# Kernel tuning notes

Hardware: AMD Instinct MI355X
Metric: run time of the kernel (lower is better)

Reference implementation:

```python
import jax, jax.numpy as jnp
import numpy as np

N_SRC = 50000
N_DST = 50000
E = 800000
IN_DIM = 128
OUT_DIM = 64
HEADS = 4
NEG_SLOPE = 0.2  # PyG GATConv default negative_slope
EPS = 1e-16      # PyG softmax denominator epsilon


def setup_inputs() -> dict:
    key = jax.random.key(0)
    ks = jax.random.split(key, 8)
    x_src = jax.random.normal(ks[0], (N_SRC, IN_DIM), dtype=jnp.float32)
    x_dst = jax.random.normal(ks[1], (N_DST, IN_DIM), dtype=jnp.float32)
    src = jax.random.randint(ks[2], (E,), 0, N_SRC, dtype=jnp.int32)
    dst = jax.random.randint(ks[3], (E,), 0, N_DST, dtype=jnp.int32)
    edge_index = jnp.stack([src, dst], axis=0)
    W_src = jax.random.normal(ks[4], (IN_DIM, HEADS * OUT_DIM), dtype=jnp.float32) / np.sqrt(IN_DIM)
    W_dst = jax.random.normal(ks[5], (IN_DIM, HEADS * OUT_DIM), dtype=jnp.float32) / np.sqrt(IN_DIM)
    att_src = jax.random.normal(ks[6], (HEADS, OUT_DIM), dtype=jnp.float32) / np.sqrt(OUT_DIM)
    att_dst = jax.random.normal(ks[7], (HEADS, OUT_DIM), dtype=jnp.float32) / np.sqrt(OUT_DIM)
    bias = jnp.zeros((OUT_DIM,), dtype=jnp.float32)
    return {"x_src": x_src, "x_dst": x_dst, "edge_index": edge_index,
            "W_src": W_src, "W_dst": W_dst, "att_src": att_src,
            "att_dst": att_dst, "bias": bias}


def reference(x_src, x_dst, edge_index, W_src, W_dst, att_src, att_dst, bias):
    # Linear projections -> [N, H, C]
    hs = (x_src @ W_src).reshape(N_SRC, HEADS, OUT_DIM)
    hd = (x_dst @ W_dst).reshape(N_DST, HEADS, OUT_DIM)
    # Per-node attention logits -> [N, H]
    a_s = jnp.einsum('nhc,hc->nh', hs, att_src)
    a_d = jnp.einsum('nhc,hc->nh', hd, att_dst)

    src, dst = edge_index[0], edge_index[1]
    # Per-edge logits [E, H]
    alpha = jax.nn.leaky_relu(a_s[src] + a_d[dst], negative_slope=NEG_SLOPE)
    # Segment softmax over edges sharing the same dst node
    amax = jax.ops.segment_max(alpha, dst, num_segments=N_DST)
    alpha = jnp.exp(alpha - amax[dst])
    denom = jax.ops.segment_sum(alpha, dst, num_segments=N_DST)
    alpha = alpha / (denom[dst] + EPS)
    # (dropout=0 / eval mode: no attention dropout)
    # Message + scatter-add aggregation: out[i] = sum_e alpha_e * hs[src_e]
    msg = hs[src] * alpha[:, :, None]                 # [E, H, C]
    out = jax.ops.segment_sum(msg, dst, num_segments=N_DST)  # [N_dst, H, C]
    # concat=False -> mean over heads, then bias
    return out.mean(axis=1) + bias
```

## Files before the change

kernel.cpp:

```cpp
#include <hip/hip_runtime.h>
#include <hip/hip_bf16.h>

#define N_SRC 50000
#define N_DST 50000
#define NEDGE 800000
#define IND   128
#define HEADS 4
#define CDIM  64
#define HC    256
#define MAXDEG 96
#define NB_ALPHA 12500
#define NB_HIST  3125

typedef _Float16 half8  __attribute__((ext_vector_type(8)));
typedef _Float16 half2t __attribute__((ext_vector_type(2)));
typedef float    f32x4  __attribute__((ext_vector_type(4)));

static __device__ __forceinline__ unsigned int pack2h(float a, float b) {
    union { half2t h; unsigned int u; } v;
    v.h[0] = (_Float16)a; v.h[1] = (_Float16)b;
    return v.u;
}
static __device__ __forceinline__ half2t bits2h(unsigned int u) {
    union { unsigned int u; half2t h; } v; v.u = u; return v.h;
}

__global__ void prep_kernel(const float* __restrict__ Wdst,
                            const float* __restrict__ att_d,
                            float* __restrict__ WdA,
                            const float* __restrict__ Wsrc,
                            _Float16* __restrict__ WhT, int* __restrict__ deg) {
    int b = blockIdx.x, tid = threadIdx.x;
    if (b < 196) {
        int i = b * 256 + tid;
        if (i < N_DST) deg[i] = 0;
    } else if (b < 198) {
        int id = (b - 196) * 256 + tid;
        int k = id >> 2, h = id & 3;
        float acc = 0.f;
        for (int c = 0; c < CDIM; ++c)
            acc += Wdst[k * HC + h * CDIM + c] * att_d[h * CDIM + c];
        WdA[id] = acc;
    } else {
        int idx = (b - 198) * 256 + tid;
        int n = idx >> 7, k = idx & 127;
        WhT[idx] = (_Float16)Wsrc[k * HC + n];
    }
}

__global__ __launch_bounds__(256) void gemm_mfma_kernel(
        const float* __restrict__ x, const _Float16* __restrict__ WhT,
        const float* __restrict__ att_s,
        unsigned short* __restrict__ hsTh, float* __restrict__ a_s) {
    int tid = threadIdx.x;
    int w = tid >> 6, lane = tid & 63;
    int ll = lane & 15, q = lane >> 4;
    int rbase = blockIdx.x * 64 + w * 16;

    int arow = rbase + ll;
    if (arow >= N_SRC) arow = N_SRC - 1;
    const float* xr = x + (size_t)arow * IND + q * 8;
    half8 afrag[4];
    #pragma unroll
    for (int kf = 0; kf < 4; ++kf) {
        float4 u0 = *(const float4*)(xr + kf * 32);
        float4 u1 = *(const float4*)(xr + kf * 32 + 4);
        half8 a;
        a[0] = (_Float16)u0.x; a[1] = (_Float16)u0.y;
        a[2] = (_Float16)u0.z; a[3] = (_Float16)u0.w;
        a[4] = (_Float16)u1.x; a[5] = (_Float16)u1.y;
        a[6] = (_Float16)u1.z; a[7] = (_Float16)u1.w;
        afrag[kf] = a;
    }

    f32x4 acc[16];
    #pragma unroll
    for (int t = 0; t < 16; ++t) acc[t] = (f32x4){0.f, 0.f, 0.f, 0.f};

    #pragma unroll
    for (int t = 0; t < 16; ++t) {
        const _Float16* bp = WhT + (size_t)(t * 16 + ll) * IND + q * 8;
        half8 b0 = *(const half8*)(bp + 0);
        half8 b1 = *(const half8*)(bp + 32);
        half8 b2 = *(const half8*)(bp + 64);
        half8 b3 = *(const half8*)(bp + 96);
        f32x4 c = acc[t];
        c = __builtin_amdgcn_mfma_f32_16x16x32_f16(afrag[0], b0, c, 0, 0, 0);
        c = __builtin_amdgcn_mfma_f32_16x16x32_f16(afrag[1], b1, c, 0, 0, 0);
        c = __builtin_amdgcn_mfma_f32_16x16x32_f16(afrag[2], b2, c, 0, 0, 0);
        c = __builtin_amdgcn_mfma_f32_16x16x32_f16(afrag[3], b3, c, 0, 0, 0);
        acc[t] = c;
    }

    #pragma unroll
    for (int tg = 0; tg < 4; ++tg) {
        #pragma unroll
        for (int r = 0; r < 4; ++r) {
            int n = rbase + q * 4 + r;
            if (n < N_SRC) {
                uint2 v;
                v.x = pack2h(acc[tg     ][r], acc[tg + 4 ][r]);
                v.y = pack2h(acc[tg + 8 ][r], acc[tg + 12][r]);
                *(uint2*)(hsTh + (size_t)n * HC + (tg * 16 + ll) * 4) = v;
            }
        }
    }

    float attv[16];
    #pragma unroll
    for (int t = 0; t < 16; ++t) attv[t] = att_s[t * 16 + ll];
    #pragma unroll
    for (int r = 0; r < 4; ++r) {
        float4 p;
        p.x = acc[0][r]*attv[0]  + acc[1][r]*attv[1]  + acc[2][r]*attv[2]  + acc[3][r]*attv[3];
        p.y = acc[4][r]*attv[4]  + acc[5][r]*attv[5]  + acc[6][r]*attv[6]  + acc[7][r]*attv[7];
        p.z = acc[8][r]*attv[8]  + acc[9][r]*attv[9]  + acc[10][r]*attv[10]+ acc[11][r]*attv[11];
        p.w = acc[12][r]*attv[12]+ acc[13][r]*attv[13]+ acc[14][r]*attv[14]+ acc[15][r]*attv[15];
        #pragma unroll
        for (int off = 1; off < 16; off <<= 1) {
            p.x += __shfl_xor(p.x, off, 64);
            p.y += __shfl_xor(p.y, off, 64);
            p.z += __shfl_xor(p.z, off, 64);
            p.w += __shfl_xor(p.w, off, 64);
        }
        int n = rbase + q * 4 + r;
        if (ll == 0 && n < N_SRC) *(float4*)(a_s + (size_t)n * 4) = p;
    }
}

__global__ __launch_bounds__(256) void mid_kernel(
        const float* __restrict__ x_dst, const float* __restrict__ WdA,
        float* __restrict__ a_d,
        const int* __restrict__ src, const int* __restrict__ dst,
        int* __restrict__ deg, int* __restrict__ col2) {
    int b = blockIdx.x, tid = threadIdx.x;
    if (b < NB_ALPHA) {
        int n    = (b * 256 + tid) >> 6;
        int lane = tid & 63;
        const float* xp = x_dst + (size_t)n * IND;
        const float4* wa = (const float4*)WdA;
        float x0 = xp[lane], x1 = xp[lane + 64];
        float4 wa0 = wa[lane], wa1 = wa[lane + 64];
        float p0 = x0 * wa0.x + x1 * wa1.x;
        float p1 = x0 * wa0.y + x1 * wa1.y;
        float p2 = x0 * wa0.z + x1 * wa1.z;
        float p3 = x0 * wa0.w + x1 * wa1.w;
        for (int off = 32; off >= 1; off >>= 1) {
            p0 += __shfl_xor(p0, off, 64);
            p1 += __shfl_xor(p1, off, 64);
            p2 += __shfl_xor(p2, off, 64);
            p3 += __shfl_xor(p3, off, 64);
        }
        if (lane == 0) {
            a_d[n * 4 + 0] = p0; a_d[n * 4 + 1] = p1;
            a_d[n * 4 + 2] = p2; a_d[n * 4 + 3] = p3;
        }
    } else {
        int e = (b - NB_ALPHA) * 256 + tid;
        if (e < NEDGE) {
            int d = dst[e];
            int r = atomicAdd(&deg[d], 1);
            if (r < MAXDEG) col2[d * MAXDEG + r] = src[e];
        }
    }
}

__global__ __launch_bounds__(256) void aggregate_kernel(
        const int* __restrict__ deg, const int* __restrict__ col2,
        const float4* __restrict__ as4, const float4* __restrict__ ad4,
        const unsigned short* __restrict__ hsTh,
        const float* __restrict__ bias, float* __restrict__ out) {
    __shared__ int   s_off[4][MAXDEG];
    __shared__ uint4 s_pk[4][MAXDEG];
    int tid = threadIdx.x;
    int wv = tid >> 6, lane = tid & 63;
    int i = (blockIdx.x * 256 + tid) >> 6;
    if (i >= N_DST) return;
    int dg = deg[i]; if (dg > MAXDEG) dg = MAXDEG;
    float bv = bias[lane];
    if (dg == 0) { out[i * CDIM + lane] = bv; return; }
    float4 ad = ad4[i];
    const int* crow = col2 + i * MAXDEG;

    float s0 = 0.f, s1 = 0.f, s2 = 0.f, s3 = 0.f;
    for (int e = lane; e < dg; e += 64) {
        int sn = crow[e];
        float4 av = as4[sn];
        float lx = av.x + ad.x; lx = lx > 0.f ? lx : 0.2f * lx;
        float ly = av.y + ad.y; ly = ly > 0.f ? ly : 0.2f * ly;
        float lz = av.z + ad.z; lz = lz > 0.f ? lz : 0.2f * lz;
        float lw = av.w + ad.w; lw = lw > 0.f ? lw : 0.2f * lw;
        float w0 = __expf(lx), w1 = __expf(ly), w2 = __expf(lz), w3 = __expf(lw);
        s0 += w0; s1 += w1; s2 += w2; s3 += w3;
        s_off[wv][e] = sn * HC;
        float4 wf = {w0, w1, w2, w3};
        *(float4*)&s_pk[wv][e] = wf;
    }
    for (int off = 32; off >= 1; off >>= 1) {
        s0 += __shfl_xor(s0, off, 64);
        s1 += __shfl_xor(s1, off, 64);
        s2 += __shfl_xor(s2, off, 64);
        s3 += __shfl_xor(s3, off, 64);
    }
    float i0 = 0.25f / (s0 + 1e-16f);
    float i1 = 0.25f / (s1 + 1e-16f);
    float i2 = 0.25f / (s2 + 1e-16f);
    float i3 = 0.25f / (s3 + 1e-16f);

    for (int e = lane; e < dg; e += 64) {
        float4 wf = *(float4*)&s_pk[wv][e];
        uint4 pk;
        pk.x = (unsigned int)s_off[wv][e];
        pk.y = pack2h(wf.x * i0, wf.y * i1);
        pk.z = pack2h(wf.z * i2, wf.w * i3);
        pk.w = 0;
        s_pk[wv][e] = pk;
    }
    __asm__ volatile("s_waitcnt lgkmcnt(0)" ::: "memory");

    const unsigned short* hb = hsTh + (lane << 2);
    float acc = 0.f;
    int j = 0;
    for (; j + 4 <= dg; j += 4) {
        uint4 p0 = s_pk[wv][j];
        uint4 p1 = s_pk[wv][j + 1];
        uint4 p2 = s_pk[wv][j + 2];
        uint4 p3 = s_pk[wv][j + 3];
        uint2 h0 = *(const uint2*)(hb + p0.x);
        uint2 h1 = *(const uint2*)(hb + p1.x);
        uint2 h2 = *(const uint2*)(hb + p2.x);
        uint2 h3 = *(const uint2*)(hb + p3.x);
        acc = __builtin_amdgcn_fdot2(bits2h(h0.x), bits2h(p0.y), acc, false);
        acc = __builtin_amdgcn_fdot2(bits2h(h0.y), bits2h(p0.z), acc, false);
        acc = __builtin_amdgcn_fdot2(bits2h(h1.x), bits2h(p1.y), acc, false);
        acc = __builtin_amdgcn_fdot2(bits2h(h1.y), bits2h(p1.z), acc, false);
        acc = __builtin_amdgcn_fdot2(bits2h(h2.x), bits2h(p2.y), acc, false);
        acc = __builtin_amdgcn_fdot2(bits2h(h2.y), bits2h(p2.z), acc, false);
        acc = __builtin_amdgcn_fdot2(bits2h(h3.x), bits2h(p3.y), acc, false);
        acc = __builtin_amdgcn_fdot2(bits2h(h3.y), bits2h(p3.z), acc, false);
    }
    for (; j < dg; ++j) {
        uint4 p0 = s_pk[wv][j];
        uint2 h0 = *(const uint2*)(hb + p0.x);
        acc = __builtin_amdgcn_fdot2(bits2h(h0.x), bits2h(p0.y), acc, false);
        acc = __builtin_amdgcn_fdot2(bits2h(h0.y), bits2h(p0.z), acc, false);
    }
    out[i * CDIM + lane] = acc + bv;
}

extern "C" void kernel_launch(void* const* d_in, const int* in_sizes, int n_in,
                              void* d_out, int out_size, void* d_ws, size_t ws_size,
                              hipStream_t stream) {
    const float* x_src   = (const float*)d_in[0];
    const float* x_dst   = (const float*)d_in[1];
    const int*   ei      = (const int*)d_in[2];
    const float* W_src   = (const float*)d_in[3];
    const float* W_dst   = (const float*)d_in[4];
    const float* att_src = (const float*)d_in[5];
    const float* att_dst = (const float*)d_in[6];
    const float* bias    = (const float*)d_in[7];
    float* out = (float*)d_out;

    char* ws = (char*)d_ws;
    unsigned short* hsTh = (unsigned short*)ws; ws += (size_t)N_SRC * HC * 2;
    int*    col2    = (int*)ws;    ws += (size_t)N_DST * MAXDEG * 4;
    float*  a_s     = (float*)ws;  ws += (size_t)N_SRC * 4 * 4;
    float*  a_d     = (float*)ws;  ws += (size_t)N_DST * 4 * 4;
    float*  WdA     = (float*)ws;  ws += 2048;
    _Float16* WhT   = (_Float16*)ws; ws += IND * HC * 2;
    int*    deg     = (int*)ws;    ws += N_DST * 4;

    prep_kernel<<<326, 256, 0, stream>>>(W_dst, att_dst, WdA, W_src, WhT, deg);
    gemm_mfma_kernel<<<(N_SRC + 63) / 64, 256, 0, stream>>>(x_src, WhT, att_src, hsTh, a_s);
    mid_kernel<<<NB_ALPHA + NB_HIST, 256, 0, stream>>>(x_dst, WdA, a_d, ei, ei + NEDGE, deg, col2);
    aggregate_kernel<<<(N_DST + 3) / 4, 256, 0, stream>>>(deg, col2,
                                                          (const float4*)a_s, (const float4*)a_d,
                                                          hsTh, bias, out);
}
```

Before: 251.5 us.

## Fuse GEMM with alpha/histogram kernel, partition scatter by dst range, shrink col indices

Merges the source-projection GEMM and the dst-logit/bucketing kernel into one launch, which removes a launch and lets the two phases overlap. The edge bucketing is split into 8 dst-range partitions: every edge chunk is read 8 times, but each block only touches one eighth of the deg/col arrays, so the scattered atomics and stores stay more local in cache. Column indices are stored as 16-bit values, halving the bucket footprint. The aggregate kernel orders its blocks to match the partitions. The a_d computation now does two nodes per wave. The risk is the 8x redundant reading of dst indices.

```diff
diff --git a/kernel.cpp b/kernel.cpp
--- a/kernel.cpp
+++ b/kernel.cpp
@@ -9,8 +9,12 @@
 #define CDIM  64
 #define HC    256
 #define MAXDEG 96
-#define NB_ALPHA 12500
-#define NB_HIST  3125
+#define NDST8 6250
+
+#define NB_GEMM  782
+#define NB_ALPHA 6250
+#define NB_HIST  25000
+#define NB_AGG   (1563 * 8)
 
 typedef _Float16 half8  __attribute__((ext_vector_type(8)));
 typedef _Float16 half2t __attribute__((ext_vector_type(2)));
@@ -48,125 +52,126 @@
     }
 }
 
-__global__ __launch_bounds__(256) void gemm_mfma_kernel(
-        const float* __restrict__ x, const _Float16* __restrict__ WhT,
+__global__ __launch_bounds__(256) void fused_kernel(
+        const float* __restrict__ x_src, const _Float16* __restrict__ WhT,
         const float* __restrict__ att_s,
-        unsigned short* __restrict__ hsTh, float* __restrict__ a_s) {
-    int tid = threadIdx.x;
-    int w = tid >> 6, lane = tid & 63;
-    int ll = lane & 15, q = lane >> 4;
-    int rbase = blockIdx.x * 64 + w * 16;
-
-    int arow = rbase + ll;
-    if (arow >= N_SRC) arow = N_SRC - 1;
-    const float* xr = x + (size_t)arow * IND + q * 8;
-    half8 afrag[4];
-    #pragma unroll
-    for (int kf = 0; kf < 4; ++kf) {
-        float4 u0 = *(const float4*)(xr + kf * 32);
-        float4 u1 = *(const float4*)(xr + kf * 32 + 4);
-        half8 a;
-        a[0] = (_Float16)u0.x; a[1] = (_Float16)u0.y;
-        a[2] = (_Float16)u0.z; a[3] = (_Float16)u0.w;
-        a[4] = (_Float16)u1.x; a[5] = (_Float16)u1.y;
-        a[6] = (_Float16)u1.z; a[7] = (_Float16)u1.w;
-        afrag[kf] = a;
-    }
-
-    f32x4 acc[16];
-    #pragma unroll
-    for (int t = 0; t < 16; ++t) acc[t] = (f32x4){0.f, 0.f, 0.f, 0.f};
-
-    #pragma unroll
-    for (int t = 0; t < 16; ++t) {
-        const _Float16* bp = WhT + (size_t)(t * 16 + ll) * IND + q * 8;
-        half8 b0 = *(const half8*)(bp + 0);
-        half8 b1 = *(const half8*)(bp + 32);
-        half8 b2 = *(const half8*)(bp + 64);
-        half8 b3 = *(const half8*)(bp + 96);
-        f32x4 c = acc[t];
-        c = __builtin_amdgcn_mfma_f32_16x16x32_f16(afrag[0], b0, c, 0, 0, 0);
-        c = __builtin_amdgcn_mfma_f32_16x16x32_f16(afrag[1], b1, c, 0, 0, 0);
-        c = __builtin_amdgcn_mfma_f32_16x16x32_f16(afrag[2], b2, c, 0, 0, 0);
-        c = __builtin_amdgcn_mfma_f32_16x16x32_f16(afrag[3], b3, c, 0, 0, 0);
-        acc[t] = c;
-    }
-
-    #pragma unroll
-    for (int tg = 0; tg < 4; ++tg) {
-        #pragma unroll
-        for (int r = 0; r < 4; ++r) {
-            int n = rbase + q * 4 + r;
-            if (n < N_SRC) {
-                uint2 v;
-                v.x = pack2h(acc[tg     ][r], acc[tg + 4 ][r]);
-                v.y = pack2h(acc[tg + 8 ][r], acc[tg + 12][r]);
-                *(uint2*)(hsTh + (size_t)n * HC + (tg * 16 + ll) * 4) = v;
-            }
-        }
-    }
-
-    float attv[16];
-    #pragma unroll
-    for (int t = 0; t < 16; ++t) attv[t] = att_s[t * 16 + ll];
-    #pragma unroll
-    for (int r = 0; r < 4; ++r) {
-        float4 p;
-        p.x = acc[0][r]*attv[0]  + acc[1][r]*attv[1]  + acc[2][r]*attv[2]  + acc[3][r]*attv[3];
-        p.y = acc[4][r]*attv[4]  + acc[5][r]*attv[5]  + acc[6][r]*attv[6]  + acc[7][r]*attv[7];
-        p.z = acc[8][r]*attv[8]  + acc[9][r]*attv[9]  + acc[10][r]*attv[10]+ acc[11][r]*attv[11];
-        p.w = acc[12][r]*attv[12]+ acc[13][r]*attv[13]+ acc[14][r]*attv[14]+ acc[15][r]*attv[15];
-        #pragma unroll
-        for (int off = 1; off < 16; off <<= 1) {
-            p.x += __shfl_xor(p.x, off, 64);
-            p.y += __shfl_xor(p.y, off, 64);
-            p.z += __shfl_xor(p.z, off, 64);
-            p.w += __shfl_xor(p.w, off, 64);
-        }
-        int n = rbase + q * 4 + r;
-        if (ll == 0 && n < N_SRC) *(float4*)(a_s + (size_t)n * 4) = p;
-    }
-}
-
-__global__ __launch_bounds__(256) void mid_kernel(
+        unsigned short* __restrict__ hsTh, float* __restrict__ a_s,
         const float* __restrict__ x_dst, const float* __restrict__ WdA,
         float* __restrict__ a_d,
         const int* __restrict__ src, const int* __restrict__ dst,
-        int* __restrict__ deg, int* __restrict__ col2) {
+        int* __restrict__ deg, unsigned short* __restrict__ col2u) {
     int b = blockIdx.x, tid = threadIdx.x;
-    if (b < NB_ALPHA) {
-        int n    = (b * 256 + tid) >> 6;
-        int lane = tid & 63;
-        const float* xp = x_dst + (size_t)n * IND;
+    int wv = tid >> 6, lane = tid & 63;
+
+    if (b < NB_GEMM) {
+        int ll = lane & 15, q = lane >> 4;
+        int rbase = b * 64 + wv * 16;
+        int arow = rbase + ll;
+        if (arow >= N_SRC) arow = N_SRC - 1;
+        const float* xr = x_src + (size_t)arow * IND + q * 8;
+        half8 afrag[4];
+        #pragma unroll
+        for (int kf = 0; kf < 4; ++kf) {
+            float4 u0 = *(const float4*)(xr + kf * 32);
+            float4 u1 = *(const float4*)(xr + kf * 32 + 4);
+            half8 a;
+            a[0] = (_Float16)u0.x; a[1] = (_Float16)u0.y;
+            a[2] = (_Float16)u0.z; a[3] = (_Float16)u0.w;
+            a[4] = (_Float16)u1.x; a[5] = (_Float16)u1.y;
+            a[6] = (_Float16)u1.z; a[7] = (_Float16)u1.w;
+            afrag[kf] = a;
+        }
+        f32x4 acc[16];
+        #pragma unroll
+        for (int t = 0; t < 16; ++t) acc[t] = (f32x4){0.f, 0.f, 0.f, 0.f};
+        #pragma unroll
+        for (int t = 0; t < 16; ++t) {
+            const _Float16* bp = WhT + (size_t)(t * 16 + ll) * IND + q * 8;
+            half8 b0 = *(const half8*)(bp + 0);
+            half8 b1 = *(const half8*)(bp + 32);
+            half8 b2 = *(const half8*)(bp + 64);
+            half8 b3 = *(const half8*)(bp + 96);
+            f32x4 c = acc[t];
+            c = __builtin_amdgcn_mfma_f32_16x16x32_f16(afrag[0], b0, c, 0, 0, 0);
+            c = __builtin_amdgcn_mfma_f32_16x16x32_f16(afrag[1], b1, c, 0, 0, 0);
+            c = __builtin_amdgcn_mfma_f32_16x16x32_f16(afrag[2], b2, c, 0, 0, 0);
+            c = __builtin_amdgcn_mfma_f32_16x16x32_f16(afrag[3], b3, c, 0, 0, 0);
+            acc[t] = c;
+        }
+        #pragma unroll
+        for (int tg = 0; tg < 4; ++tg) {
+            #pragma unroll
+            for (int r = 0; r < 4; ++r) {
+                int n = rbase + q * 4 + r;
+                if (n < N_SRC) {
+                    uint2 v;
+                    v.x = pack2h(acc[tg     ][r], acc[tg + 4 ][r]);
+                    v.y = pack2h(acc[tg + 8 ][r], acc[tg + 12][r]);
+                    *(uint2*)(hsTh + (size_t)n * HC + (tg * 16 + ll) * 4) = v;
+                }
+            }
+        }
+        float attv[16];
+        #pragma unroll
+        for (int t = 0; t < 16; ++t) attv[t] = att_s[t * 16 + ll];
+        #pragma unroll
+        for (int r = 0; r < 4; ++r) {
+            float4 p;
+            p.x = acc[0][r]*attv[0]  + acc[1][r]*attv[1]  + acc[2][r]*attv[2]  + acc[3][r]*attv[3];
+            p.y = acc[4][r]*attv[4]  + acc[5][r]*attv[5]  + acc[6][r]*attv[6]  + acc[7][r]*attv[7];
+            p.z = acc[8][r]*attv[8]  + acc[9][r]*attv[9]  + acc[10][r]*attv[10]+ acc[11][r]*attv[11];
+            p.w = acc[12][r]*attv[12]+ acc[13][r]*attv[13]+ acc[14][r]*attv[14]+ acc[15][r]*attv[15];
+            #pragma unroll
+            for (int off = 1; off < 16; off <<= 1) {
+                p.x += __shfl_xor(p.x, off, 64);
+                p.y += __shfl_xor(p.y, off, 64);
+                p.z += __shfl_xor(p.z, off, 64);
+                p.w += __shfl_xor(p.w, off, 64);
+            }
+            int n = rbase + q * 4 + r;
+            if (ll == 0 && n < N_SRC) *(float4*)(a_s + (size_t)n * 4) = p;
+        }
+    } else if (b < NB_GEMM + NB_ALPHA) {
+        int base = (b - NB_GEMM) * 8 + wv * 2;
         const float4* wa = (const float4*)WdA;
-        float x0 = xp[lane], x1 = xp[lane + 64];
         float4 wa0 = wa[lane], wa1 = wa[lane + 64];
-        float p0 = x0 * wa0.x + x1 * wa1.x;
-        float p1 = x0 * wa0.y + x1 * wa1.y;
-        float p2 = x0 * wa0.z + x1 * wa1.z;
-        float p3 = x0 * wa0.w + x1 * wa1.w;
-        for (int off = 32; off >= 1; off >>= 1) {
-            p0 += __shfl_xor(p0, off, 64);
-            p1 += __shfl_xor(p1, off, 64);
-            p2 += __shfl_xor(p2, off, 64);
-            p3 += __shfl_xor(p3, off, 64);
-        }
-        if (lane == 0) {
-            a_d[n * 4 + 0] = p0; a_d[n * 4 + 1] = p1;
-            a_d[n * 4 + 2] = p2; a_d[n * 4 + 3] = p3;
+        #pragma unroll
+        for (int k = 0; k < 2; ++k) {
+            int n = base + k;
+            const float* xp = x_dst + (size_t)n * IND;
+            float x0 = xp[lane], x1 = xp[lane + 64];
+            float p0 = x0 * wa0.x + x1 * wa1.x;
+            float p1 = x0 * wa0.y + x1 * wa1.y;
+            float p2 = x0 * wa0.z + x1 * wa1.z;
+            float p3 = x0 * wa0.w + x1 * wa1.w;
+            for (int off = 32; off >= 1; off >>= 1) {
+                p0 += __shfl_xor(p0, off, 64);
+                p1 += __shfl_xor(p1, off, 64);
+                p2 += __shfl_xor(p2, off, 64);
+                p3 += __shfl_xor(p3, off, 64);
+            }
+            if (lane == 0) {
+                a_d[n * 4 + 0] = p0; a_d[n * 4 + 1] = p1;
+                a_d[n * 4 + 2] = p2; a_d[n * 4 + 3] = p3;
+            }
         }
     } else {
-        int e = (b - NB_ALPHA) * 256 + tid;
+        int b2 = b - (NB_GEMM + NB_ALPHA);
+        int chunk = b2 >> 3;
+        int part  = b2 & 7;
+        int e = chunk * 256 + tid;
         if (e < NEDGE) {
             int d = dst[e];
-            int r = atomicAdd(&deg[d], 1);
-            if (r < MAXDEG) col2[d * MAXDEG + r] = src[e];
+            if ((unsigned)(d - part * NDST8) < NDST8) {
+                int r = atomicAdd(&deg[d], 1);
+                if (r < MAXDEG) col2u[d * MAXDEG + r] = (unsigned short)src[e];
+            }
         }
     }
 }
 
 __global__ __launch_bounds__(256) void aggregate_kernel(
-        const int* __restrict__ deg, const int* __restrict__ col2,
+        const int* __restrict__ deg, const unsigned short* __restrict__ col2u,
         const float4* __restrict__ as4, const float4* __restrict__ ad4,
         const unsigned short* __restrict__ hsTh,
         const float* __restrict__ bias, float* __restrict__ out) {
@@ -174,13 +179,15 @@
     __shared__ uint4 s_pk[4][MAXDEG];
     int tid = threadIdx.x;
     int wv = tid >> 6, lane = tid & 63;
-    int i = (blockIdx.x * 256 + tid) >> 6;
-    if (i >= N_DST) return;
+    int part = blockIdx.x & 7;
+    int loc  = (blockIdx.x >> 3) * 4 + wv;
+    if (loc >= NDST8) return;
+    int i = part * NDST8 + loc;
     int dg = deg[i]; if (dg > MAXDEG) dg = MAXDEG;
     float bv = bias[lane];
     if (dg == 0) { out[i * CDIM + lane] = bv; return; }
     float4 ad = ad4[i];
-    const int* crow = col2 + i * MAXDEG;
+    const unsigned short* crow = col2u + i * MAXDEG;
 
     float s0 = 0.f, s1 = 0.f, s2 = 0.f, s3 = 0.f;
     for (int e = lane; e < dg; e += 64) {
@@ -263,7 +270,7 @@
 
     char* ws = (char*)d_ws;
     unsigned short* hsTh = (unsigned short*)ws; ws += (size_t)N_SRC * HC * 2;
-    int*    col2    = (int*)ws;    ws += (size_t)N_DST * MAXDEG * 4;
+    unsigned short* col2u = (unsigned short*)ws; ws += (size_t)N_DST * MAXDEG * 2;
     float*  a_s     = (float*)ws;  ws += (size_t)N_SRC * 4 * 4;
     float*  a_d     = (float*)ws;  ws += (size_t)N_DST * 4 * 4;
     float*  WdA     = (float*)ws;  ws += 2048;
@@ -271,9 +278,11 @@
     int*    deg     = (int*)ws;    ws += N_DST * 4;
 
     prep_kernel<<<326, 256, 0, stream>>>(W_dst, att_dst, WdA, W_src, WhT, deg);
-    gemm_mfma_kernel<<<(N_SRC + 63) / 64, 256, 0, stream>>>(x_src, WhT, att_src, hsTh, a_s);
-    mid_kernel<<<NB_ALPHA + NB_HIST, 256, 0, stream>>>(x_dst, WdA, a_d, ei, ei + NEDGE, deg, col2);
-    aggregate_kernel<<<(N_DST + 3) / 4, 256, 0, stream>>>(deg, col2,
-                                                          (const float4*)a_s, (const float4*)a_d,
-                                                          hsTh, bias, out);
-}
+    fused_kernel<<<NB_GEMM + NB_ALPHA + NB_HIST, 256, 0, stream>>>(
+        x_src, WhT, att_src, hsTh, a_s,
+        x_dst, WdA, a_d,
+        ei, ei + NEDGE, deg, col2u);
+    aggregate_kernel<<<NB_AGG, 256, 0, stream>>>(deg, col2u,
+                                                 (const float4*)a_s, (const float4*)a_d,
+                                                 hsTh, bias, out);
+}
```

Result: slower. 263.9 us (+4.9%).
